# Kernel tuning notes

Measured on AMD Instinct MI355X. Metric: run time of the kernel, lower is better.

## Reference

```python
import jax, jax.numpy as jnp
import numpy as np

N, D, HW, FF, DD = 128, 256, 28, 2048, 64
NP_ = D * DD  # num_params = hidden_dim * dim_dynamic = 16384
NH_SELF, NH_ENC = 8, 4


def _conv(x, w, b, stride=1):
    y = jax.lax.conv_general_dilated(x, w, (stride, stride), ((1, 1), (1, 1)),
                                     dimension_numbers=('NCHW', 'OIHW', 'NCHW'))
    return y + b[None, :, None, None]


def _bn(x, g, b):
    # eval-mode BatchNorm2d with running_mean=0, running_var=1
    return x * g[None, :, None, None] + b[None, :, None, None]


def _ln(x, g, b, eps=1e-5):
    m = x.mean(-1, keepdims=True)
    v = ((x - m) ** 2).mean(-1, keepdims=True)
    return (x - m) / jnp.sqrt(v + eps) * g + b


def _mha(x, qkv_w, qkv_b, out_w, out_b, nh):
    # x: (S, B, D) seq-first, like torch MultiheadAttention
    S, B, Dm = x.shape
    dh = Dm // nh
    q, k, v = jnp.split(x @ qkv_w.T + qkv_b, 3, axis=-1)
    q = q.reshape(S, B, nh, dh) * (1.0 / np.sqrt(dh))
    k = k.reshape(S, B, nh, dh)
    v = v.reshape(S, B, nh, dh)
    a = jax.nn.softmax(jnp.einsum('sbhd,tbhd->bhst', q, k), axis=-1)
    o = jnp.einsum('bhst,tbhd->sbhd', a, v).reshape(S, B, Dm)
    return o @ out_w.T + out_b


def _up2(x):
    return jnp.repeat(jnp.repeat(x, 2, axis=2), 2, axis=3)


def _pe(max_len, d):
    pos = jnp.arange(max_len, dtype=jnp.float32)[:, None]
    div = jnp.exp(jnp.arange(0, d, 2, dtype=jnp.float32) * (-np.log(10000.0) / d))
    pe = jnp.zeros((max_len, d), jnp.float32)
    pe = pe.at[:, 0::2].set(jnp.sin(pos * div)).at[:, 1::2].set(jnp.cos(pos * div))
    return pe[:, None, :]  # (max_len, 1, d)


def _forward(roi_features, pro_features, enc_conv_w, enc_conv_b, enc_bn_g, enc_bn_b, attn_qkv_w, attn_qkv_b, attn_out_w, attn_out_b, norm1_g, norm1_b, norm2_g, norm2_b, norm3_g, norm3_b, dyn_w, dyn_b, dnorm1_g, dnorm1_b, dnorm2_g, dnorm2_b, lin1_w, lin1_b, lin2_w, lin2_b, te_qkv_w, te_qkv_b, te_out_w, te_out_b, te_ln1_g, te_ln1_b, te_ln2_g, te_ln2_b, te_ff1_w, te_ff1_b, te_ff2_w, te_ff2_b, rec_conv_w, rec_conv_b, rec_bn_g, rec_bn_b, detA_w, detA_b, det_bnA_g, det_bnA_b, detB_w, detB_b, det_final_w, det_final_b, det_final_bn_g, det_final_bn_b):
    n = roi_features.shape[0]
    h4 = HW // 4
    # ---- k_encoder: two stride-2 conv+BN+ReLU, 28->14->7 ----
    feats_pyr = []
    k = roi_features
    for i in range(2):
        k = jax.nn.relu(_bn(_conv(k, enc_conv_w[i], enc_conv_b[i], stride=2), enc_bn_g[i], enc_bn_b[i]))
        feats_pyr.append(k)
    k = k.reshape(n, D, h4 * h4).transpose(2, 0, 1)  # (49, N, D)
    # ---- self-attention over query tokens ----
    pro = pro_features.reshape(-1, pro_features.shape[-2], D).transpose(1, 0, 2)  # (nq, bs*nf, D)
    pro = _ln(pro + _mha(pro, attn_qkv_w, attn_qkv_b, attn_out_w, attn_out_b, NH_SELF), norm1_g, norm1_b)
    pro = pro.transpose(1, 0, 2).reshape(1, -1, D)  # (1, N, D)
    # ---- DynamicConv_v2 instance interaction ----
    feats = k.transpose(1, 0, 2)  # (N, 49, D)
    params = (pro @ dyn_w.T + dyn_b).transpose(1, 0, 2)  # (N, 1, 2*NP_)
    p1 = params[:, :, :NP_].reshape(-1, D, DD)   # (N, D, 64)
    p2 = params[:, :, NP_:].reshape(-1, DD, D)   # (N, 64, D)
    f = jax.nn.elu(_ln(jnp.einsum('nsc,ncd->nsd', feats, p1), dnorm1_g, dnorm1_b))
    f = jax.nn.elu(_ln(jnp.einsum('nsd,ndc->nsc', f, p2), dnorm2_g, dnorm2_b))  # (N, 49, D)
    pro = feats + f
    obj = _ln(pro, norm2_g, norm2_b)
    # ---- FFN (ELU activation) ----
    obj2 = jax.nn.elu(obj @ lin1_w.T + lin1_b) @ lin2_w.T + lin2_b
    obj = _ln(obj + obj2, norm3_g, norm3_b)
    # ---- pos encoding + 3-layer TransformerEncoder (post-norm, relu, nhead=4) ----
    obj = obj.transpose(1, 0, 2)  # (49, N, D)
    obj = obj + _pe(h4 * h4, D)
    for l in range(3):
        a = _mha(obj, te_qkv_w[l], te_qkv_b[l], te_out_w[l], te_out_b[l], NH_ENC)
        obj = _ln(obj + a, te_ln1_g[l], te_ln1_b[l])
        ff = jax.nn.relu(obj @ te_ff1_w[l].T + te_ff1_b[l]) @ te_ff2_w[l].T + te_ff2_b[l]
        obj = _ln(obj + ff, te_ln2_g[l], te_ln2_b[l])
    obj = obj.transpose(1, 2, 0).reshape(n, D, h4, h4)
    kmap = k.transpose(1, 2, 0).reshape(n, D, h4, h4)
    # ---- gated rec/det decoder pyramid ----
    k_rec = kmap * jax.nn.sigmoid(obj)
    k_rec = jax.nn.relu(_bn(_conv(_up2(k_rec), rec_conv_w[0], rec_conv_b[0]), rec_bn_g[0], rec_bn_b[0])) + feats_pyr[0]
    k_det = _conv(jax.nn.relu(_bn(_conv(_up2(obj), detA_w[0], detA_b[0]), det_bnA_g[0], det_bnA_b[0])), detB_w[0], detB_b[0]) + feats_pyr[0]
    k_rec = k_rec * jax.nn.sigmoid(k_det)
    k_rec = jax.nn.relu(_bn(_conv(_up2(k_rec), rec_conv_w[1], rec_conv_b[1]), rec_bn_g[1], rec_bn_b[1])) + roi_features
    k_det = _conv(jax.nn.relu(_bn(_conv(_up2(k_det), detA_w[1], detA_b[1]), det_bnA_g[1], det_bnA_b[1])), detB_w[1], detB_b[1]) + roi_features
    k_rec = k_rec * jax.nn.sigmoid(k_det)
    # final decoder_layer: Upsample to (28,28) is identity here, then conv+BN+ReLU
    k_rec = jax.nn.relu(_bn(_conv(k_rec, det_final_w, det_final_b), det_final_bn_g, det_final_bn_b))
    return k_rec.reshape(n, D, HW * HW).transpose(0, 2, 1)  # (N, 784, D)


def setup_inputs():
    keys = iter(jax.random.split(jax.random.key(0), 80))
    def rn(shape, s=0.02):
        return jax.random.normal(next(keys), shape, jnp.float32) * s
    d = {
        'roi_features': jax.random.normal(next(keys), (N, D, HW, HW), jnp.float32),
        'pro_features': jax.random.normal(next(keys), (1, 1, N, D), jnp.float32),
        'gt_masks': jax.random.normal(next(keys), (N, HW, HW), jnp.float32),
        'enc_conv_w': rn((2, D, D, 3, 3)), 'enc_conv_b': rn((2, D)),
        'enc_bn_g': jnp.ones((2, D)), 'enc_bn_b': jnp.zeros((2, D)),
        'attn_qkv_w': rn((3 * D, D)), 'attn_qkv_b': rn((3 * D,)),
        'attn_out_w': rn((D, D)), 'attn_out_b': rn((D,)),
        'norm1_g': jnp.ones((D,)), 'norm1_b': jnp.zeros((D,)),
        'norm2_g': jnp.ones((D,)), 'norm2_b': jnp.zeros((D,)),
        'norm3_g': jnp.ones((D,)), 'norm3_b': jnp.zeros((D,)),
        'dyn_w': rn((2 * NP_, D)), 'dyn_b': rn((2 * NP_,)),
        'dnorm1_g': jnp.ones((DD,)), 'dnorm1_b': jnp.zeros((DD,)),
        'dnorm2_g': jnp.ones((D,)), 'dnorm2_b': jnp.zeros((D,)),
        'lin1_w': rn((FF, D)), 'lin1_b': rn((FF,)),
        'lin2_w': rn((D, FF)), 'lin2_b': rn((D,)),
        'te_qkv_w': rn((3, 3 * D, D)), 'te_qkv_b': rn((3, 3 * D)),
        'te_out_w': rn((3, D, D)), 'te_out_b': rn((3, D)),
        'te_ln1_g': jnp.ones((3, D)), 'te_ln1_b': jnp.zeros((3, D)),
        'te_ln2_g': jnp.ones((3, D)), 'te_ln2_b': jnp.zeros((3, D)),
        'te_ff1_w': rn((3, FF, D)), 'te_ff1_b': rn((3, FF)),
        'te_ff2_w': rn((3, D, FF)), 'te_ff2_b': rn((3, D)),
        'rec_conv_w': rn((2, D, D, 3, 3)), 'rec_conv_b': rn((2, D)),
        'rec_bn_g': jnp.ones((2, D)), 'rec_bn_b': jnp.zeros((2, D)),
        'detA_w': rn((2, D, D, 3, 3)), 'detA_b': rn((2, D)),
        'det_bnA_g': jnp.ones((2, D)), 'det_bnA_b': jnp.zeros((2, D)),
        'detB_w': rn((2, D, D, 3, 3)), 'detB_b': rn((2, D)),
        'det_final_w': rn((D, D, 3, 3)), 'det_final_b': rn((D,)),
        'det_final_bn_g': jnp.ones((D,)), 'det_final_bn_b': jnp.zeros((D,)),
    }
    return d


def reference(roi_features, pro_features, gt_masks, enc_conv_w, enc_conv_b, enc_bn_g, enc_bn_b, attn_qkv_w, attn_qkv_b, attn_out_w, attn_out_b, norm1_g, norm1_b, norm2_g, norm2_b, norm3_g, norm3_b, dyn_w, dyn_b, dnorm1_g, dnorm1_b, dnorm2_g, dnorm2_b, lin1_w, lin1_b, lin2_w, lin2_b, te_qkv_w, te_qkv_b, te_out_w, te_out_b, te_ln1_g, te_ln1_b, te_ln2_g, te_ln2_b, te_ff1_w, te_ff1_b, te_ff2_w, te_ff2_b, rec_conv_w, rec_conv_b, rec_bn_g, rec_bn_b, detA_w, detA_b, det_bnA_g, det_bnA_b, detB_w, detB_b, det_final_w, det_final_b, det_final_bn_g, det_final_bn_b):
    # gt_masks is only consumed by the (truncated) SequencePredictor head; unused here
    return _forward(roi_features, pro_features, enc_conv_w, enc_conv_b, enc_bn_g, enc_bn_b, attn_qkv_w, attn_qkv_b, attn_out_w, attn_out_b, norm1_g, norm1_b, norm2_g, norm2_b, norm3_g, norm3_b, dyn_w, dyn_b, dnorm1_g, dnorm1_b, dnorm2_g, dnorm2_b, lin1_w, lin1_b, lin2_w, lin2_b, te_qkv_w, te_qkv_b, te_out_w, te_out_b, te_ln1_g, te_ln1_b, te_ln2_g, te_ln2_b, te_ff1_w, te_ff1_b, te_ff2_w, te_ff2_b, rec_conv_w, rec_conv_b, rec_bn_g, rec_bn_b, detA_w, detA_b, det_bnA_g, det_bnA_b, detB_w, detB_b, det_final_w, det_final_b, det_final_bn_g, det_final_bn_b)
```

## Files before the change

### kernel.cpp

```cpp
#include <hip/hip_runtime.h>
#include <hip/hip_bf16.h>
#include <string.h>

typedef __hip_bfloat16 bf16;
typedef short bf16x8 __attribute__((ext_vector_type(8)));
typedef float f32x16 __attribute__((ext_vector_type(16)));

typedef __attribute__((address_space(3))) unsigned int       as3_u32;
typedef const __attribute__((address_space(1))) unsigned int as1_u32c;

__device__ __forceinline__ void dma16(const void* g, void* l){
  __builtin_amdgcn_global_load_lds((as1_u32c*)g, (as3_u32*)l, 16, 0, 0);
}

__device__ __align__(256) unsigned char g_zpad[1024];

__device__ __forceinline__ float b2f(bf16 v){ return __bfloat162float(v); }
__device__ __forceinline__ bf16  f2b(float v){ return __float2bfloat16(v); }
__device__ __forceinline__ unsigned short f2bu(float v){
  union { bf16 b; unsigned short u; } x; x.b = __float2bfloat16(v); return x.u;
}
__device__ __forceinline__ float ldf(const float* p, size_t i){ return p[i]; }
__device__ __forceinline__ float ldf(const bf16*  p, size_t i){ return b2f(p[i]); }

__device__ __forceinline__ int xcd_swizzle(int lin, int nwg){
  int q = nwg >> 3, r = nwg & 7;
  int x = lin & 7, i = lin >> 3;
  int base = (x < r) ? x * (q + 1) : r * (q + 1) + (x - r) * q;
  return base + i;
}

__device__ __forceinline__ float2 block_stats256(float x, float* sred){
  float v = x;
  #pragma unroll
  for (int o = 32; o; o >>= 1) v += __shfl_xor(v, o);
  int w = threadIdx.x >> 6;
  if ((threadIdx.x & 63) == 0) sred[w] = v;
  __syncthreads();
  float mean = (sred[0] + sred[1] + sred[2] + sred[3]) * (1.f/256.f);
  __syncthreads();
  float d = x - mean;
  v = d * d;
  #pragma unroll
  for (int o = 32; o; o >>= 1) v += __shfl_xor(v, o);
  if ((threadIdx.x & 63) == 0) sred[w] = v;
  __syncthreads();
  float var = (sred[0] + sred[1] + sred[2] + sred[3]) * (1.f/256.f);
  __syncthreads();
  return make_float2(mean, var);
}

__global__ __launch_bounds__(256) void probe_k(const bf16* __restrict__ buf,
                                               unsigned long long len, float* score){
  __shared__ float sred[4];
  unsigned long long stride = len / 256ull; if (!stride) stride = 1;
  unsigned long long i = (unsigned long long)threadIdx.x * stride;
  if (i >= len) i = len - 1;
  float v = fabsf(b2f(buf[i]));
  #pragma unroll
  for (int o = 32; o; o >>= 1) v = fmaxf(v, __shfl_xor(v, o));
  if ((threadIdx.x & 63) == 0) sred[threadIdx.x >> 6] = v;
  __syncthreads();
  if (threadIdx.x == 0)
    score[0] = fmaxf(fmaxf(sred[0], sred[1]), fmaxf(sred[2], sred[3]));
}

__global__ void verdict_k(const float* score, int nstage, float* out){
  if (threadIdx.x == 0 && blockIdx.x == 0){
    for (int i = 0; i < nstage; i++){
      float s = score[i];
      if (!(s > 1e-8f)){
        float sent = 1000.f + 40.f * i;
        for (int j = 0; j < 64; j++) out[j] = sent;
        return;
      }
    }
  }
}

__global__ __launch_bounds__(256) void cvt_k(const float* __restrict__ s,
                                             bf16* __restrict__ d, int n4){
  int i = blockIdx.x * 256 + threadIdx.x;
  if (i < n4){
    float4 f = reinterpret_cast<const float4*>(s)[i];
    ushort4 u;
    u.x = f2bu(f.x); u.y = f2bu(f.y); u.z = f2bu(f.z); u.w = f2bu(f.w);
    reinterpret_cast<ushort4*>(d)[i] = u;
  }
}

__global__ __launch_bounds__(256) void troi_k(const float* __restrict__ roi,
                                              bf16* __restrict__ o){
  __shared__ float tile[64][65];
  int n = blockIdx.z, c0 = blockIdx.y * 64, p0 = blockIdx.x * 64;
  int a = threadIdx.x & 63, bq = threadIdx.x >> 6;
  #pragma unroll
  for (int cs = bq; cs < 64; cs += 4){
    int p = p0 + a;
    tile[cs][a] = (p < 784) ? roi[((size_t)n*256 + c0 + cs)*784 + p] : 0.f;
  }
  __syncthreads();
  #pragma unroll
  for (int ps = bq; ps < 64; ps += 4){
    int p = p0 + ps;
    if (p < 784) o[((size_t)n*784 + p)*256 + c0 + a] = f2b(tile[a][ps]);
  }
}

__global__ __launch_bounds__(256) void wtrans_k(const float* __restrict__ w,
                                                bf16* __restrict__ o){
  int co = blockIdx.x, t = threadIdx.x;
  const float* wp = w + (size_t)co * 2304 + (size_t)t * 9;
  #pragma unroll
  for (int tap = 0; tap < 9; tap++)
    o[(size_t)co * 2304 + tap * 256 + t] = f2b(wp[tap]);
}

__device__ __forceinline__ void mfma_step64(const unsigned short* As,
                                            const unsigned short* Bs,
                                            int wr, int wc, int lane,
                                            f32x16 (&acc)[2][2]){
  const char* asb = (const char*)As;
  const char* bsb = (const char*)Bs;
  int l31 = lane & 31;
  int lsw = (l31 & 7) << 4;
  int hi  = (lane >> 5) << 4;
  #pragma unroll
  for (int kb = 0; kb < 4; kb++){
    int cb = (kb*32 + hi) ^ lsw;
    bf16x8 a0 = *reinterpret_cast<const bf16x8*>(asb + (wr      + l31)*128 + cb);
    bf16x8 a1 = *reinterpret_cast<const bf16x8*>(asb + (wr + 32 + l31)*128 + cb);
    bf16x8 b0 = *reinterpret_cast<const bf16x8*>(bsb + (wc      + l31)*128 + cb);
    bf16x8 b1 = *reinterpret_cast<const bf16x8*>(bsb + (wc + 32 + l31)*128 + cb);
    acc[0][0] = __builtin_amdgcn_mfma_f32_32x32x16_bf16(a0, b0, acc[0][0], 0, 0, 0);
    acc[0][1] = __builtin_amdgcn_mfma_f32_32x32x16_bf16(a0, b1, acc[0][1], 0, 0, 0);
    acc[1][0] = __builtin_amdgcn_mfma_f32_32x32x16_bf16(a1, b0, acc[1][0], 0, 0, 0);
    acc[1][1] = __builtin_amdgcn_mfma_f32_32x32x16_bf16(a1, b1, acc[1][1], 0, 0, 0);
  }
}

template<int ACT>
__global__ __launch_bounds__(256) void gemm_mfma_k(
    const bf16* __restrict__ A, const bf16* __restrict__ W,
    const float* __restrict__ bias, bf16* __restrict__ C,
    int M, int N, int K)
{
  __shared__ __align__(16) unsigned short As[2][8192];
  __shared__ __align__(16) unsigned short Bs[2][8192];
  int t = threadIdx.x;
  int nbx = gridDim.x;
  int lin = blockIdx.y * nbx + blockIdx.x;
  int wg  = xcd_swizzle(lin, nbx * gridDim.y);
  int n0 = (wg % nbx) * 128, m0 = (wg / nbx) * 128;
  int lane = t & 63, wave = t >> 6;
  int wr = (wave >> 1) * 64, wc = (wave & 1) * 64;
  int lrow = lane >> 3;
  int e0   = (((lane & 7) ^ lrow) << 3);

  f32x16 acc[2][2];
  #pragma unroll
  for (int i = 0; i < 2; i++)
    #pragma unroll
    for (int j = 0; j < 2; j++)
      #pragma unroll
      for (int r = 0; r < 16; r++) acc[i][j][r] = 0.f;

  const bf16* apr[4]; const bf16* bpr[4];
  #pragma unroll
  for (int i = 0; i < 4; i++){
    int r = wave*32 + i*8 + lrow;
    apr[i] = A + (size_t)(m0 + r) * K + e0;
    bpr[i] = W + (size_t)(n0 + r) * K + e0;
  }

  auto stage = [&](int buf, int k0){
    #pragma unroll
    for (int i = 0; i < 4; i++){
      dma16(apr[i] + k0, &As[buf][(wave*32 + i*8) * 64]);
      dma16(bpr[i] + k0, &Bs[buf][(wave*32 + i*8) * 64]);
    }
  };

  int NIT = K >> 6;
  stage(0, 0);
  __syncthreads();
  #pragma unroll 1
  for (int it = 0; it < NIT; ++it){
    if (it + 1 < NIT) stage((it+1)&1, (it+1)*64);
    mfma_step64(As[it&1], Bs[it&1], wr, wc, lane, acc);
    __syncthreads();
  }

  int l31 = lane & 31;
  int rbase = m0 + wr + ((lane >> 5) << 2);
  #pragma unroll
  for (int j = 0; j < 2; j++){
    int n = n0 + wc + j*32 + l31;
    float bv = bias ? bias[n] : 0.f;
    #pragma unroll
    for (int i = 0; i < 2; i++){
      #pragma unroll
      for (int r = 0; r < 16; r++){
        int row = rbase + i*32 + (r & 3) + ((r >> 2) << 3);
        float v = acc[i][j][r] + bv;
        if (ACT == 1) v = fmaxf(v, 0.f);
        if (ACT == 2) v = v > 0.f ? v : (__expf(v) - 1.f);
        C[(size_t)row * N + n] = f2b(v);
      }
    }
  }
}

template<int Ho,int Wo,int Hi,int Wi,int UP2,int STRIDE,
         int HAS_BN,int RELU,int RES_MODE,int GATE,int WOUT,int OUTF>
__global__ __launch_bounds__(256) void conv_mfma_k(
    const bf16* __restrict__ in, const bf16* __restrict__ wTl,
    const float* __restrict__ cbias,
    const float* __restrict__ bng, const float* __restrict__ bnb,
    const void* __restrict__ res, bf16* __restrict__ gate,
    void* __restrict__ out)
{
  constexpr int HWo = Ho * Wo;
  constexpr int Hv = UP2 ? 2*Hi : Hi;
  constexpr int Wv = UP2 ? 2*Wi : Wi;
  __shared__ __align__(16) unsigned short As[2][8192];
  __shared__ __align__(16) unsigned short Bs[2][8192];
  int t = threadIdx.x;
  int nbx = gridDim.x;
  int lin = blockIdx.y * nbx + blockIdx.x;
  int wg  = xcd_swizzle(lin, nbx * gridDim.y);
  int co0 = (wg % nbx) * 128;
  int gp0 = (wg / nbx) * 128;
  int lane = t & 63, wave = t >> 6;
  int wr = (wave >> 1) * 64, wc = (wave & 1) * 64;
  int lrow = lane >> 3;
  int e0   = (((lane & 7) ^ lrow) << 3);

  int nA[4], oyA[4], oxA[4]; size_t wbase[4];
  #pragma unroll
  for (int i = 0; i < 4; i++){
    int r  = wave*32 + i*8 + lrow;
    int gp = gp0 + r;
    nA[i] = gp / HWo;
    int p = gp - nA[i] * HWo;
    oyA[i] = p / Wo; oxA[i] = p - oyA[i] * Wo;
    wbase[i] = (size_t)(co0 + r) * 2304 + e0;
  }

  f32x16 acc[2][2];
  #pragma unroll
  for (int i = 0; i < 2; i++)
    #pragma unroll
    for (int j = 0; j < 2; j++)
      #pragma unroll
      for (int r = 0; r < 16; r++) acc[i][j][r] = 0.f;

  const bf16* arp[4]; const bf16* brp[4];

  auto stage = [&](int buf, int it){
    int tap = it >> 2, sub = it & 3;
    if (sub == 0){
      int ky = tap / 3, kx = tap - ky * 3;
      #pragma unroll
      for (int i = 0; i < 4; i++){
        int iy = oyA[i]*STRIDE + ky - 1;
        int ix = oxA[i]*STRIDE + kx - 1;
        bool val = (iy >= 0) && (iy < Hv) && (ix >= 0) && (ix < Wv);
        int sy = UP2 ? (iy >> 1) : iy;
        int sx = UP2 ? (ix >> 1) : ix;
        arp[i] = val
          ? in + (((size_t)nA[i] * Hi + sy) * Wi + sx) * 256 + e0
          : (const bf16*)g_zpad + e0;
        brp[i] = wTl + wbase[i] + tap*256;
      }
    }
    #pragma unroll
    for (int i = 0; i < 4; i++){
      dma16(arp[i] + sub*64, &As[buf][(wave*32 + i*8) * 64]);
      dma16(brp[i] + sub*64, &Bs[buf][(wave*32 + i*8) * 64]);
    }
  };

  stage(0, 0);
  __syncthreads();
  #pragma unroll 1
  for (int it = 0; it < 36; ++it){
    if (it + 1 < 36) stage((it+1)&1, it+1);
    mfma_step64(As[it&1], Bs[it&1], wr, wc, lane, acc);
    __syncthreads();
  }

  int l31 = lane & 31;
  int rbase = gp0 + wr + ((lane >> 5) << 2);
  #pragma unroll
  for (int j = 0; j < 2; j++){
    int co = co0 + wc + j*32 + l31;
    float cb = cbias[co];
    float scale = 1.f, shift = cb;
    if (HAS_BN){ float g = bng[co]; scale = g; shift = cb*g + bnb[co]; }
    #pragma unroll
    for (int i = 0; i < 2; i++){
      #pragma unroll
      for (int r = 0; r < 16; r++){
        int grow = rbase + i*32 + (r & 3) + ((r >> 2) << 3);
        float v = acc[i][j][r] * scale + shift;
        if (RELU) v = fmaxf(v, 0.f);
        size_t oidx = (size_t)grow * 256 + co;
        if (RES_MODE == 1) v += b2f(((const bf16*)res)[oidx]);
        if (RES_MODE == 2){
          int rn = grow / HWo, rp = grow - rn * HWo;
          v += ((const float*)res)[((size_t)rn * 256 + co) * HWo + rp];
        }
        if (GATE){
          float gv = b2f(gate[oidx]);
          gate[oidx] = f2b(gv / (1.f + __expf(-v)));
        }
        if (WOUT){
          if (OUTF) ((float*)out)[oidx] = v;
          else      ((bf16*)out)[oidx]  = f2b(v);
        }
      }
    }
  }
}

template<int S, int NH, int DH>
__global__ __launch_bounds__(64) void attn_k(
    const bf16* __restrict__ qkv, bf16* __restrict__ out)
{
  const int D = NH * DH;
  int b = blockIdx.x / NH, h = blockIdx.x % NH;
  int chunk = blockIdx.y;
  int lane = threadIdx.x;
  __shared__ float ks[S][DH];
  __shared__ float vs[S][DH];
  __shared__ float os[64][DH];
  for (int idx = lane; idx < S*DH; idx += 64){
    int tt = idx / DH, d = idx % DH;
    size_t row = (size_t)(b*S + tt) * (3*D);
    ks[tt][d] = b2f(qkv[row +   D + h*DH + d]);
    vs[tt][d] = b2f(qkv[row + 2*D + h*DH + d]);
  }
  __syncthreads();
  int s = chunk*64 + lane;
  float q[DH];
  const float scale = 1.f / sqrtf((float)DH);
  if (s < S){
    size_t row = (size_t)(b*S + s) * (3*D);
    #pragma unroll
    for (int d = 0; d < DH; d++) q[d] = b2f(qkv[row + h*DH + d]) * scale;
  } else {
    #pragma unroll
    for (int d = 0; d < DH; d++) q[d] = 0.f;
  }
  float o[DH];
  #pragma unroll
  for (int d = 0; d < DH; d++) o[d] = 0.f;
  float m = -1e30f, l = 0.f;
  for (int tt = 0; tt < S; tt++){
    float sc = 0.f;
    #pragma unroll
    for (int d = 0; d < DH; d++) sc = fmaf(q[d], ks[tt][d], sc);
    float mn = fmaxf(m, sc);
    float corr = __expf(m - mn);
    float e = __expf(sc - mn);
    l = l * corr + e;
    #pragma unroll
    for (int d = 0; d < DH; d++) o[d] = fmaf(o[d], corr, e * vs[tt][d]);
    m = mn;
  }
  float inv = 1.f / l;
  #pragma unroll
  for (int d = 0; d < DH; d++) os[lane][d] = o[d] * inv;
  __syncthreads();
  for (int idx = lane; idx < 64*DH; idx += 64){
    int sl = idx / DH, d = idx % DH;
    int ss = chunk*64 + sl;
    if (ss < S) out[(size_t)(b*S + ss) * D + h*DH + d] = f2b(os[sl][d]);
  }
}

template<int ADD_PE, typename TA>
__global__ __launch_bounds__(256) void add_ln_k(
    const TA* __restrict__ a, const bf16* __restrict__ bsrc,
    const float* __restrict__ g, const float* __restrict__ bb, bf16* out)
{
  __shared__ float sred[4];
  int r = blockIdx.x, c = threadIdx.x;
  size_t idx = (size_t)r * 256 + c;
  float x = ldf(a, idx) + b2f(bsrc[idx]);
  float2 mv = block_stats256(x, sred);
  float y = (x - mv.x) * rsqrtf(mv.y + 1e-5f) * g[c] + bb[c];
  if (ADD_PE){
    int s = r % 49;
    float freq = __expf((float)(c & ~1) * (-9.210340371976184f / 256.f));
    float ang = (float)s * freq;
    y += (c & 1) ? cosf(ang) : sinf(ang);
  }
  out[idx] = f2b(y);
}

__global__ __launch_bounds__(256) void dyn_e1_k(
    const bf16* __restrict__ k2, const bf16* __restrict__ params,
    const float* __restrict__ g, const float* __restrict__ bb,
    bf16* __restrict__ f1)
{
  int n = blockIdx.x;
  int w = threadIdx.x >> 6, d = threadIdx.x & 63;
  const bf16* pp = params + (size_t)n * 32768 + d;
  for (int s = w; s < 49; s += 4){
    const bf16* fp = k2 + ((size_t)n*49 + s) * 256;
    float acc = 0.f;
    #pragma unroll 4
    for (int c = 0; c < 256; c++)
      acc = fmaf(b2f(fp[c]), b2f(pp[c*64]), acc);
    float v = acc;
    #pragma unroll
    for (int o = 32; o; o >>= 1) v += __shfl_xor(v, o);
    float mean = v * (1.f/64.f);
    float dd = acc - mean;
    v = dd * dd;
    #pragma unroll
    for (int o = 32; o; o >>= 1) v += __shfl_xor(v, o);
    float var = v * (1.f/64.f);
    float y = dd * rsqrtf(var + 1e-5f) * g[d] + bb[d];
    y = y > 0.f ? y : (__expf(y) - 1.f);
    f1[((size_t)n*49 + s) * 64 + d] = f2b(y);
  }
}

__global__ __launch_bounds__(256) void dyn_e2_k(
    const bf16* __restrict__ k2, const bf16* __restrict__ params,
    const bf16* __restrict__ f1,
    const float* __restrict__ g2, const float* __restrict__ bb2,
    const float* __restrict__ ng, const float* __restrict__ nb,
    bf16* __restrict__ obj0)
{
  __shared__ float sred[4];
  int ns = blockIdx.x; int n = ns / 49, s = ns % 49;
  int c = threadIdx.x;
  const bf16* pp  = params + (size_t)n * 32768 + 16384 + c;
  const bf16* f1p = f1 + (size_t)ns * 64;
  float acc = 0.f;
  #pragma unroll 8
  for (int d = 0; d < 64; d++)
    acc = fmaf(b2f(f1p[d]), b2f(pp[d*256]), acc);
  float2 mv = block_stats256(acc, sred);
  float y = (acc - mv.x) * rsqrtf(mv.y + 1e-5f) * g2[c] + bb2[c];
  y = y > 0.f ? y : (__expf(y) - 1.f);
  float pro2 = b2f(k2[((size_t)n*49 + s) * 256 + c]) + y;
  float2 mv2 = block_stats256(pro2, sred);
  float y2 = (pro2 - mv2.x) * rsqrtf(mv2.y + 1e-5f) * ng[c] + nb[c];
  obj0[(size_t)ns * 256 + c] = f2b(y2);
}

__global__ __launch_bounds__(256) void gate7_k(
    const bf16* __restrict__ k2, const bf16* __restrict__ obj,
    bf16* __restrict__ rec7)
{
  size_t idx = (size_t)blockIdx.x * 256 + threadIdx.x;
  float ov = b2f(obj[idx]);
  rec7[idx] = f2b(b2f(k2[idx]) / (1.f + __expf(-ov)));
}

extern "C" void kernel_launch(void* const* d_in, const int* in_sizes, int n_in,
                              void* d_out, int out_size, void* d_ws, size_t ws_size,
                              hipStream_t stream)
{
  (void)hipGetLastError();

  static float h_sent[64];
  auto send_sentinel = [&](float val){
    for (int i = 0; i < 64; i++) h_sent[i] = val;
    hipMemcpyAsync(d_out, h_sent, 256, hipMemcpyHostToDevice, stream);
  };

  static const int EXP_SIZES[53] = {
    25690112, 32768, 100352, 1179648, 512, 512, 512, 196608, 768, 65536,
    256, 256, 256, 256, 256, 256, 256, 8388608, 32768, 64,
    64, 256, 256, 524288, 2048, 524288, 256, 589824, 2304, 196608,
    768, 768, 768, 768, 768, 1572864, 6144, 1572864, 768, 1179648,
    512, 512, 512, 1179648, 512, 512, 512, 1179648, 512, 589824,
    256, 256, 256 };
  if (n_in != 53){ send_sentinel(6600.f + (float)n_in); return; }
  for (int i = 0; i < 53; i++)
    if (in_sizes[i] != EXP_SIZES[i]){ send_sentinel(6000.f + 10.f*i); return; }
  if (out_size != 25690112){ send_sentinel(3000.f + (float)(out_size >> 20)); return; }
  if (ws_size < 77070400ull){ send_sentinel(2000.f + (float)(ws_size >> 20)); return; }

  const float* roi    = (const float*)d_in[0];
  const float* proF   = (const float*)d_in[1];
  const float* encW   = (const float*)d_in[3];
  const float* encB   = (const float*)d_in[4];
  const float* encG   = (const float*)d_in[5];
  const float* encBB  = (const float*)d_in[6];
  const float* aqkvW  = (const float*)d_in[7];
  const float* aqkvB  = (const float*)d_in[8];
  const float* aoutW  = (const float*)d_in[9];
  const float* aoutB  = (const float*)d_in[10];
  const float* n1g    = (const float*)d_in[11];
  const float* n1b    = (const float*)d_in[12];
  const float* n2g    = (const float*)d_in[13];
  const float* n2b    = (const float*)d_in[14];
  const float* n3g    = (const float*)d_in[15];
  const float* n3b    = (const float*)d_in[16];
  const float* dynW   = (const float*)d_in[17];
  const float* dynB   = (const float*)d_in[18];
  const float* dn1g   = (const float*)d_in[19];
  const float* dn1b   = (const float*)d_in[20];
  const float* dn2g   = (const float*)d_in[21];
  const float* dn2b   = (const float*)d_in[22];
  const float* lin1W  = (const float*)d_in[23];
  const float* lin1B  = (const float*)d_in[24];
  const float* lin2W  = (const float*)d_in[25];
  const float* lin2B  = (const float*)d_in[26];
  const float* teqkvW = (const float*)d_in[27];
  const float* teqkvB = (const float*)d_in[28];
  const float* teoutW = (const float*)d_in[29];
  const float* teoutB = (const float*)d_in[30];
  const float* teln1g = (const float*)d_in[31];
  const float* teln1b = (const float*)d_in[32];
  const float* teln2g = (const float*)d_in[33];
  const float* teln2b = (const float*)d_in[34];
  const float* teff1W = (const float*)d_in[35];
  const float* teff1B = (const float*)d_in[36];
  const float* teff2W = (const float*)d_in[37];
  const float* teff2B = (const float*)d_in[38];
  const float* recW   = (const float*)d_in[39];
  const float* recB   = (const float*)d_in[40];
  const float* recG   = (const float*)d_in[41];
  const float* recBB  = (const float*)d_in[42];
  const float* dAW    = (const float*)d_in[43];
  const float* dAB    = (const float*)d_in[44];
  const float* dAG    = (const float*)d_in[45];
  const float* dABB   = (const float*)d_in[46];
  const float* dBW    = (const float*)d_in[47];
  const float* dBB_   = (const float*)d_in[48];
  const float* dfW    = (const float*)d_in[49];
  const float* dfB    = (const float*)d_in[50];
  const float* dfG    = (const float*)d_in[51];
  const float* dfBB   = (const float*)d_in[52];

  bf16* base   = (bf16*)d_ws;
  bf16* wT     = base + 0;
  bf16* k1     = base + 5308416;
  bf16* k2     = base + 11730944;
  bf16* qkvP   = base + 13336576;
  bf16* attoP  = base + 13434880;
  bf16* mhaP   = base + 13467648;
  bf16* proQ   = base + 13500416;
  bf16* f1     = base + 13533184;
  bf16* obj0   = base + 13934592;
  bf16* tmp    = base + 15540224;
  bf16* atto   = base + 17145856;
  bf16* obj    = base + 18751488;
  bf16* params = base + 20357120;
  bf16* rec7   = base + 20357120;
  bf16* hbuf   = base + 24551424;
  bf16* qkvT   = base + 24551424;
  bf16* C14    = base + 24551424;
  bf16* B14    = base + 32112640;
  bf16* B28    = base + 5308416;
  bf16* proB   = atto;
  bf16* roiT   = (bf16*)d_out;
  bf16* C28    = (bf16*)d_out + 6422528;
  bf16* gw     = (bf16*)d_out + 26214400;
  bf16* A14    = (bf16*)d_out + 39845888;
  bf16* gqkvW  = gw + 0;
  bf16* gaoutW = gw + 196608;
  bf16* gdynW  = gw + 262144;
  bf16* glin1W = gw + 8650752;
  bf16* glin2W = gw + 9175040;
  bf16* gteqkvW= gw + 9699328;
  bf16* gteoutW= gw + 10289152;
  bf16* gteff1W= gw + 10485760;
  bf16* gteff2W= gw + 12058624;
  float* score = (float*)((char*)d_ws + 77070336);

  auto cvt = [&](const float* s, bf16* d, int n){
    cvt_k<<<(n/4 + 255)/256, 256, 0, stream>>>(s, d, n/4);
  };
  troi_k<<<dim3(13,4,128),256,0,stream>>>(roi, roiT);
  wtrans_k<<<256,256,0,stream>>>(encW,            wT + 0*589824);
  wtrans_k<<<256,256,0,stream>>>(encW + 589824,   wT + 1*589824);
  wtrans_k<<<256,256,0,stream>>>(recW,            wT + 2*589824);
  wtrans_k<<<256,256,0,stream>>>(recW + 589824,   wT + 3*589824);
  wtrans_k<<<256,256,0,stream>>>(dAW,             wT + 4*589824);
  wtrans_k<<<256,256,0,stream>>>(dAW + 589824,    wT + 5*589824);
  wtrans_k<<<256,256,0,stream>>>(dBW,             wT + 6*589824);
  wtrans_k<<<256,256,0,stream>>>(dBW + 589824,    wT + 7*589824);
  wtrans_k<<<256,256,0,stream>>>(dfW,             wT + 8*589824);
  cvt(proF,   proB,    32768);
  cvt(aqkvW,  gqkvW,   196608);
  cvt(aoutW,  gaoutW,  65536);
  cvt(dynW,   gdynW,   8388608);
  cvt(lin1W,  glin1W,  524288);
  cvt(lin2W,  glin2W,  524288);
  cvt(teqkvW, gteqkvW, 589824);
  cvt(teoutW, gteoutW, 196608);
  cvt(teff1W, gteff1W, 1572864);
  cvt(teff2W, gteff2W, 1572864);
  probe_k<<<1,256,0,stream>>>(roiT, 25690112ull, score+0);

  conv_mfma_k<14,14,28,28,0,2, 1,1,0,0,1,0><<<dim3(2,196),256,0,stream>>>(
      roiT, wT + 0*589824, encB, encG, encBB, nullptr, nullptr, k1);
  probe_k<<<1,256,0,stream>>>(k1, 6422528ull, score+1);
  conv_mfma_k<7,7,14,14,0,2, 1,1,0,0,1,0><<<dim3(2,49),256,0,stream>>>(
      k1, wT + 1*589824, encB+256, encG+256, encBB+256, nullptr, nullptr, k2);
  probe_k<<<1,256,0,stream>>>(k2, 1605632ull, score+2);

  gemm_mfma_k<0><<<dim3(6,1),256,0,stream>>>(proB, gqkvW, aqkvB, qkvP, 128,768,256);
  probe_k<<<1,256,0,stream>>>(qkvP, 98304ull, score+3);
  attn_k<128,8,32><<<dim3(8,2),64,0,stream>>>(qkvP, attoP);
  gemm_mfma_k<0><<<dim3(2,1),256,0,stream>>>(attoP, gaoutW, aoutB, mhaP, 128,256,256);
  add_ln_k<0,bf16><<<128,256,0,stream>>>(proB, mhaP, n1g, n1b, proQ);
  probe_k<<<1,256,0,stream>>>(proQ, 32768ull, score+4);

  gemm_mfma_k<0><<<dim3(256,1),256,0,stream>>>(proQ, gdynW, dynB, params, 128,32768,256);
  probe_k<<<1,256,0,stream>>>(params, 4194304ull, score+5);
  dyn_e1_k<<<128,256,0,stream>>>(k2, params, dn1g, dn1b, f1);
  probe_k<<<1,256,0,stream>>>(f1, 401408ull, score+6);
  dyn_e2_k<<<6272,256,0,stream>>>(k2, params, f1, dn2g, dn2b, n2g, n2b, obj0);
  probe_k<<<1,256,0,stream>>>(obj0, 1605632ull, score+7);

  gemm_mfma_k<2><<<dim3(16,49),256,0,stream>>>(obj0, glin1W, lin1B, hbuf, 6272,2048,256);
  gemm_mfma_k<0><<<dim3(2,49),256,0,stream>>>(hbuf, glin2W, lin2B, tmp, 6272,256,2048);
  add_ln_k<1,bf16><<<6272,256,0,stream>>>(obj0, tmp, n3g, n3b, obj);
  probe_k<<<1,256,0,stream>>>(obj, 1605632ull, score+8);

  for (int l = 0; l < 3; l++){
    gemm_mfma_k<0><<<dim3(6,49),256,0,stream>>>(
        obj, gteqkvW + (size_t)l*196608, teqkvB + l*768, qkvT, 6272,768,256);
    attn_k<49,4,64><<<dim3(512,1),64,0,stream>>>(qkvT, atto);
    gemm_mfma_k<0><<<dim3(2,49),256,0,stream>>>(
        atto, gteoutW + (size_t)l*65536, teoutB + l*256, tmp, 6272,256,256);
    add_ln_k<0,bf16><<<6272,256,0,stream>>>(obj, tmp, teln1g + l*256, teln1b + l*256, obj);
    gemm_mfma_k<1><<<dim3(16,49),256,0,stream>>>(
        obj, gteff1W + (size_t)l*524288, teff1B + l*2048, hbuf, 6272,2048,256);
    gemm_mfma_k<0><<<dim3(2,49),256,0,stream>>>(
        hbuf, gteff2W + (size_t)l*524288, teff2B + l*256, tmp, 6272,256,2048);
    add_ln_k<0,bf16><<<6272,256,0,stream>>>(obj, tmp, teln2g + l*256, teln2b + l*256, obj);
  }
  probe_k<<<1,256,0,stream>>>(obj, 1605632ull, score+9);

  gate7_k<<<6272,256,0,stream>>>(k2, obj, rec7);
  probe_k<<<1,256,0,stream>>>(rec7, 1605632ull, score+10);
  conv_mfma_k<14,14,7,7,1,1, 1,1,1,0,1,0><<<dim3(2,196),256,0,stream>>>(
      rec7, wT + 2*589824, recB, recG, recBB, k1, nullptr, B14);
  probe_k<<<1,256,0,stream>>>(B14, 6422528ull, score+11);
  conv_mfma_k<14,14,7,7,1,1, 1,1,0,0,1,0><<<dim3(2,196),256,0,stream>>>(
      obj, wT + 4*589824, dAB, dAG, dABB, nullptr, nullptr, C14);
  conv_mfma_k<14,14,14,14,0,1, 0,0,1,1,1,0><<<dim3(2,196),256,0,stream>>>(
      C14, wT + 6*589824, dBB_, nullptr, nullptr, k1, B14, A14);
  probe_k<<<1,256,0,stream>>>(A14, 6422528ull, score+12);
  conv_mfma_k<28,28,14,14,1,1, 1,1,1,0,1,0><<<dim3(2,784),256,0,stream>>>(
      B14, wT + 3*589824, recB+256, recG+256, recBB+256, roiT, nullptr, B28);
  probe_k<<<1,256,0,stream>>>(B28, 25690112ull, score+13);
  conv_mfma_k<28,28,14,14,1,1, 1,1,0,0,1,0><<<dim3(2,784),256,0,stream>>>(
      A14, wT + 5*589824, dAB+256, dAG+256, dABB+256, nullptr, nullptr, C28);
  conv_mfma_k<28,28,28,28,0,1, 0,0,2,1,0,0><<<dim3(2,784),256,0,stream>>>(
      C28, wT + 7*589824, dBB_+256, nullptr, nullptr, roi, B28, nullptr);
  conv_mfma_k<28,28,28,28,0,1, 1,1,0,0,1,1><<<dim3(2,784),256,0,stream>>>(
      B28, wT + 8*589824, dfB, dfG, dfBB, nullptr, nullptr, d_out);

  verdict_k<<<1,64,0,stream>>>(score, 14, (float*)d_out);
  hipError_t le = hipGetLastError();
  if (le != hipSuccess){
    float v = 7000.f + 16.f * (float)(int)le;
    if (v > 60000.f) v = 60000.f;
    send_sentinel(v);
  }
}
```

Baseline: 2.189 ms.

## Fold 2x nearest upsample into conv weights via sub-pixel 2x2 decomposition

A nearest-neighbour 2x upsample followed by a 3x3 conv is rewritten as four 2x2 convolutions on the low-resolution input, one per output parity. Each uses folded weights that sum the taps landing on the same source pixel, computed by a new weight-folding kernel. The new convup_k kernel runs K=1024 (4 taps x 256 channels) instead of 2304, cutting MFMA work for the four upsample convs to about 4/9. The cost is an extra weight-folding pass, scattered output writes, and weight rounding that differs slightly because taps are summed before the bf16 conversion.

```diff
diff --git a/kernel.cpp b/kernel.cpp
--- a/kernel.cpp
+++ b/kernel.cpp
@@ -114,6 +114,33 @@
   #pragma unroll
   for (int tap = 0; tap < 9; tap++)
     o[(size_t)co * 2304 + tap * 256 + t] = f2b(wp[tap]);
+}
+
+__global__ __launch_bounds__(256) void wfold_k(const float* __restrict__ w,
+                                               bf16* __restrict__ wF){
+  int co = blockIdx.x, ci = threadIdx.x;
+  float t9[9];
+  #pragma unroll
+  for (int k = 0; k < 9; k++) t9[k] = w[(size_t)co*2304 + (size_t)ci*9 + k];
+  const int msk[2][2] = {{0b001, 0b110}, {0b011, 0b100}};
+  #pragma unroll
+  for (int py = 0; py < 2; py++)
+  #pragma unroll
+  for (int px = 0; px < 2; px++){
+    int par = py*2 + px;
+    #pragma unroll
+    for (int qy = 0; qy < 2; qy++)
+    #pragma unroll
+    for (int qx = 0; qx < 2; qx++){
+      float s = 0.f;
+      #pragma unroll
+      for (int dy = 0; dy < 3; dy++) if ((msk[py][qy] >> dy) & 1)
+        #pragma unroll
+        for (int dx = 0; dx < 3; dx++) if ((msk[px][qx] >> dx) & 1)
+          s += t9[dy*3 + dx];
+      wF[(size_t)par*262144 + (size_t)co*1024 + (qy*2+qx)*256 + ci] = f2b(s);
+    }
+  }
 }
 
 __device__ __forceinline__ void mfma_step64(const unsigned short* As,
@@ -319,6 +346,109 @@
           if (OUTF) ((float*)out)[oidx] = v;
           else      ((bf16*)out)[oidx]  = f2b(v);
         }
+      }
+    }
+  }
+}
+
+template<int Ho,int Wo,int Hi,int Wi,int RES>
+__global__ __launch_bounds__(256) void convup_k(
+    const bf16* __restrict__ in, const bf16* __restrict__ wF,
+    const float* __restrict__ cbias,
+    const float* __restrict__ bng, const float* __restrict__ bnb,
+    const bf16* __restrict__ res, bf16* __restrict__ out)
+{
+  constexpr int Ty = Ho/2, Tx = Wo/2;
+  constexpr int HWt = Ty * Tx;
+  __shared__ __align__(16) unsigned short As[2][8192];
+  __shared__ __align__(16) unsigned short Bs[2][8192];
+  int t = threadIdx.x;
+  int nbx = gridDim.x;
+  int lin = blockIdx.y * nbx + blockIdx.x;
+  int wg  = xcd_swizzle(lin, nbx * gridDim.y);
+  int co0 = (wg % nbx) * 128;
+  int gb  = wg / nbx;
+  int par = gb / HWt;
+  int gp0 = (gb - par * HWt) * 128;
+  int py = par >> 1, px = par & 1;
+  int oyOff = py ? 0 : 1, oxOff = px ? 0 : 1;
+  int lane = t & 63, wave = t >> 6;
+  int wr = (wave >> 1) * 64, wc = (wave & 1) * 64;
+  int lrow = lane >> 3;
+  int e0   = (((lane & 7) ^ lrow) << 3);
+
+  int nA[4], tyA[4], txA[4]; const bf16* brp[4];
+  #pragma unroll
+  for (int i = 0; i < 4; i++){
+    int r  = wave*32 + i*8 + lrow;
+    int gp = gp0 + r;
+    nA[i] = gp / HWt;
+    int tp = gp - nA[i] * HWt;
+    tyA[i] = tp / Tx; txA[i] = tp - tyA[i] * Tx;
+    brp[i] = wF + (size_t)par*262144 + (size_t)(co0 + r)*1024 + e0;
+  }
+
+  f32x16 acc[2][2];
+  #pragma unroll
+  for (int i = 0; i < 2; i++)
+    #pragma unroll
+    for (int j = 0; j < 2; j++)
+      #pragma unroll
+      for (int r = 0; r < 16; r++) acc[i][j][r] = 0.f;
+
+  const bf16* arp[4];
+  auto stage = [&](int buf, int it){
+    int quad = it >> 2, sub = it & 3;
+    if (sub == 0){
+      int qy = quad >> 1, qx = quad & 1;
+      #pragma unroll
+      for (int i = 0; i < 4; i++){
+        int sy = tyA[i] + qy - oyOff;
+        int sx = txA[i] + qx - oxOff;
+        bool val = (sy >= 0) && (sy < Hi) && (sx >= 0) && (sx < Wi);
+        arp[i] = val
+          ? in + (((size_t)nA[i] * Hi + sy) * Wi + sx) * 256 + e0
+          : (const bf16*)g_zpad + e0;
+      }
+    }
+    #pragma unroll
+    for (int i = 0; i < 4; i++){
+      dma16(arp[i] + sub*64, &As[buf][(wave*32 + i*8) * 64]);
+      dma16(brp[i] + it*64,  &Bs[buf][(wave*32 + i*8) * 64]);
+    }
+  };
+
+  stage(0, 0);
+  __syncthreads();
+  #pragma unroll 1
+  for (int it = 0; it < 16; ++it){
+    if (it + 1 < 16) stage((it+1)&1, it+1);
+    mfma_step64(As[it&1], Bs[it&1], wr, wc, lane, acc);
+    __syncthreads();
+  }
+
+  int l31 = lane & 31;
+  int rbase = gp0 + wr + ((lane >> 5) << 2);
+  #pragma unroll
+  for (int j = 0; j < 2; j++){
+    int co = co0 + wc + j*32 + l31;
+    float cb = cbias[co];
+    float scale = 1.f, shift = cb;
+    float g = bng[co]; scale = g; shift = cb*g + bnb[co];
+    #pragma unroll
+    for (int i = 0; i < 2; i++){
+      #pragma unroll
+      for (int r = 0; r < 16; r++){
+        int grow = rbase + i*32 + (r & 3) + ((r >> 2) << 3);
+        int n  = grow / HWt;
+        int tp = grow - n * HWt;
+        int ty = tp / Tx, tx = tp - ty * Tx;
+        int oy = 2*ty + py, ox = 2*tx + px;
+        size_t oidx = (((size_t)n * Ho + oy) * Wo + ox) * 256 + co;
+        float v = acc[i][j][r] * scale + shift;
+        v = fmaxf(v, 0.f);
+        if (RES == 1) v += b2f(res[oidx]);
+        out[oidx] = f2b(v);
       }
     }
   }
@@ -566,6 +696,10 @@
   bf16* C28    = (bf16*)d_out + 6422528;
   bf16* gw     = (bf16*)d_out + 26214400;
   bf16* A14    = (bf16*)d_out + 39845888;
+  bf16* wFrec1 = (bf16*)d_out + 46268416;
+  bf16* wFrec2 = wFrec1 + 1048576;
+  bf16* wFdA1  = wFrec1 + 2097152;
+  bf16* wFdA2  = wFrec1 + 3145728;
   bf16* gqkvW  = gw + 0;
   bf16* gaoutW = gw + 196608;
   bf16* gdynW  = gw + 262144;
@@ -583,13 +717,13 @@
   troi_k<<<dim3(13,4,128),256,0,stream>>>(roi, roiT);
   wtrans_k<<<256,256,0,stream>>>(encW,            wT + 0*589824);
   wtrans_k<<<256,256,0,stream>>>(encW + 589824,   wT + 1*589824);
-  wtrans_k<<<256,256,0,stream>>>(recW,            wT + 2*589824);
-  wtrans_k<<<256,256,0,stream>>>(recW + 589824,   wT + 3*589824);
-  wtrans_k<<<256,256,0,stream>>>(dAW,             wT + 4*589824);
-  wtrans_k<<<256,256,0,stream>>>(dAW + 589824,    wT + 5*589824);
   wtrans_k<<<256,256,0,stream>>>(dBW,             wT + 6*589824);
   wtrans_k<<<256,256,0,stream>>>(dBW + 589824,    wT + 7*589824);
   wtrans_k<<<256,256,0,stream>>>(dfW,             wT + 8*589824);
+  wfold_k<<<256,256,0,stream>>>(recW,           wFrec1);
+  wfold_k<<<256,256,0,stream>>>(recW + 589824,  wFrec2);
+  wfold_k<<<256,256,0,stream>>>(dAW,            wFdA1);
+  wfold_k<<<256,256,0,stream>>>(dAW + 589824,   wFdA2);
   cvt(proF,   proB,    32768);
   cvt(aqkvW,  gqkvW,   196608);
   cvt(aoutW,  gaoutW,  65536);
@@ -645,19 +779,19 @@
 
   gate7_k<<<6272,256,0,stream>>>(k2, obj, rec7);
   probe_k<<<1,256,0,stream>>>(rec7, 1605632ull, score+10);
-  conv_mfma_k<14,14,7,7,1,1, 1,1,1,0,1,0><<<dim3(2,196),256,0,stream>>>(
-      rec7, wT + 2*589824, recB, recG, recBB, k1, nullptr, B14);
+  convup_k<14,14,7,7, 1><<<dim3(2,196),256,0,stream>>>(
+      rec7, wFrec1, recB, recG, recBB, k1, B14);
   probe_k<<<1,256,0,stream>>>(B14, 6422528ull, score+11);
-  conv_mfma_k<14,14,7,7,1,1, 1,1,0,0,1,0><<<dim3(2,196),256,0,stream>>>(
-      obj, wT + 4*589824, dAB, dAG, dABB, nullptr, nullptr, C14);
+  convup_k<14,14,7,7, 0><<<dim3(2,196),256,0,stream>>>(
+      obj, wFdA1, dAB, dAG, dABB, nullptr, C14);
   conv_mfma_k<14,14,14,14,0,1, 0,0,1,1,1,0><<<dim3(2,196),256,0,stream>>>(
       C14, wT + 6*589824, dBB_, nullptr, nullptr, k1, B14, A14);
   probe_k<<<1,256,0,stream>>>(A14, 6422528ull, score+12);
-  conv_mfma_k<28,28,14,14,1,1, 1,1,1,0,1,0><<<dim3(2,784),256,0,stream>>>(
-      B14, wT + 3*589824, recB+256, recG+256, recBB+256, roiT, nullptr, B28);
+  convup_k<28,28,14,14, 1><<<dim3(2,784),256,0,stream>>>(
+      B14, wFrec2, recB+256, recG+256, recBB+256, roiT, B28);
   probe_k<<<1,256,0,stream>>>(B28, 25690112ull, score+13);
-  conv_mfma_k<28,28,14,14,1,1, 1,1,0,0,1,0><<<dim3(2,784),256,0,stream>>>(
-      A14, wT + 5*589824, dAB+256, dAG+256, dABB+256, nullptr, nullptr, C28);
+  convup_k<28,28,14,14, 0><<<dim3(2,784),256,0,stream>>>(
+      A14, wFdA2, dAB+256, dAG+256, dABB+256, nullptr, C28);
   conv_mfma_k<28,28,28,28,0,1, 0,0,2,1,0,0><<<dim3(2,784),256,0,stream>>>(
       C28, wT + 7*589824, dBB_+256, nullptr, nullptr, roi, B28, nullptr);
   conv_mfma_k<28,28,28,28,0,1, 1,1,0,0,1,1><<<dim3(2,784),256,0,stream>>>(
```

Measured after the change: 2.030 ms. 7.3% less time.
